# Optimization experiments

Hardware: AMD Instinct MI355X
Metric: run time of the kernel (lower is better)

## Reference

```python
import jax, jax.numpy as jnp
import numpy as np

NMS_MAX_OUTPUTS = 2000
CLS_SCORE_THRESH = 0.7
IOU_THRESH = 0.3
USE_SIDE_REFINE = False
B, N_ANCHORS, N_VALID, NUM_CLASSES = 4, 20000, 12000, 2


def setup_inputs() -> dict:
    key = jax.random.key(0)
    k = jax.random.split(key, 7)
    deltas = 0.5 * jax.random.normal(k[0], (B, N_ANCHORS, 2), jnp.float32)
    side_deltas = 0.5 * jax.random.normal(k[1], (B, N_ANCHORS, 1), jnp.float32)
    class_logits = 2.0 * jax.random.normal(k[2], (B, N_ANCHORS, NUM_CLASSES), jnp.float32)
    # CTPN-style anchors: fixed width 16, heights in [11, 280], on a ~1600px page
    cx = jax.random.uniform(k[3], (N_VALID,), jnp.float32, 8.0, 1592.0)
    cy = jax.random.uniform(k[4], (N_VALID,), jnp.float32, 0.0, 1600.0)
    h = jax.random.uniform(k[5], (N_VALID,), jnp.float32, 11.0, 280.0)
    valid_anchors = jnp.stack([cx - 8.0, cy - h * 0.5, cx + 8.0, cy + h * 0.5], axis=1)
    valid_indices = jnp.sort(
        jax.random.choice(k[6], N_ANCHORS, (N_VALID,), replace=False)
    ).astype(jnp.int32)
    return {
        "deltas": deltas,
        "side_deltas": side_deltas,
        "class_logits": class_logits,
        "valid_anchors": valid_anchors,
        "valid_indices": valid_indices,
    }


def apply_regress(deltas, side_deltas, anchors, use_side_refine):
    # deltas [B,V,2], side_deltas [B,V,1], anchors [V,4] -> [B,V,4]
    w = anchors[:, 2] - anchors[:, 0]
    h = anchors[:, 3] - anchors[:, 1]
    cx = (anchors[:, 0] + anchors[:, 2]) * 0.5
    cy = (anchors[:, 1] + anchors[:, 3]) * 0.5
    d = jnp.concatenate([deltas, side_deltas], axis=-1) * jnp.array([0.1, 0.2, 0.1], deltas.dtype)
    dy, dh, dx = d[..., 0], d[..., 1], d[..., 2]
    cy = cy + dy * h
    cx = cx + dx * w
    h = h * jnp.exp(dh)
    y1 = cy - h * 0.5
    y2 = cy + h * 0.5
    if use_side_refine:
        x1 = jnp.maximum(cx - w * 0.5, 0.0)
        x2 = cx + w * 0.5
    else:
        x1 = jnp.broadcast_to(anchors[:, 0], y1.shape)
        x2 = jnp.broadcast_to(anchors[:, 2], y1.shape)
    return jnp.stack([x1, y1, x2, y2], axis=-1)


def nms_single(boxes, scores, logits, max_out, iou_t, score_t):
    """Greedy NMS (tf.image.non_max_suppression semantics) + gather + pad_to_fixed_size."""
    V = boxes.shape[0]
    order = jnp.argsort(-jax.lax.stop_gradient(scores))
    b, s, l = boxes[order], scores[order], logits[order]
    bc = jax.lax.stop_gradient(b)  # suppression decisions are non-differentiable
    x1, y1, x2, y2 = bc[:, 0], bc[:, 1], bc[:, 2], bc[:, 3]
    areas = (x2 - x1) * (y2 - y1)
    idxs = jnp.arange(V)
    valid = jax.lax.stop_gradient(s) > score_t

    def body(i, keep):
        xx1 = jnp.maximum(x1[i], x1)
        yy1 = jnp.maximum(y1[i], y1)
        xx2 = jnp.minimum(x2[i], x2)
        yy2 = jnp.minimum(y2[i], y2)
        inter = jnp.maximum(xx2 - xx1, 0.0) * jnp.maximum(yy2 - yy1, 0.0)
        iou = inter / (areas[i] + areas - inter + 1e-10)
        sup = (iou > iou_t) & (idxs > i)
        return jnp.where(keep[i], keep & ~sup, keep)

    keep = jax.lax.fori_loop(0, V, body, valid)
    rank = jnp.cumsum(keep.astype(jnp.int32)) - 1
    sel = keep & (rank < max_out)
    dest = jnp.where(sel, rank, max_out)  # overflow rows parked at row max_out, sliced off
    tag = jnp.ones((V, 1), b.dtype)

    def pad_fixed(x):
        # append tag column of 1s for real rows, scatter to fixed size, zero-pad rest
        aug = jnp.where(sel[:, None], jnp.concatenate([x, tag], axis=1), 0.0)
        out = jnp.zeros((max_out + 1, aug.shape[1]), aug.dtype).at[dest].set(aug)
        return out[:max_out]

    return pad_fixed(b), pad_fixed(s[:, None]), pad_fixed(l)


def reference(deltas, side_deltas, class_logits, valid_anchors, valid_indices):
    d = jnp.take(deltas, valid_indices, axis=1)
    sd = jnp.take(side_deltas, valid_indices, axis=1)
    cl = jnp.take(class_logits, valid_indices, axis=1)
    class_scores = jax.nn.softmax(cl, axis=-1)
    fg_scores = jnp.max(class_scores[..., 1:], axis=-1)  # [B,V]
    proposals = apply_regress(d, sd, valid_anchors, USE_SIDE_REFINE)  # [B,V,4]
    f = lambda bb, ss, ll: nms_single(bb, ss, ll, NMS_MAX_OUTPUTS, IOU_THRESH, CLS_SCORE_THRESH)
    boxes, box_scores, out_logits = jax.vmap(f)(proposals, fg_scores, cl)
    return boxes, box_scores, out_logits
```

## Files before the change

### kernel.cpp

```cpp
#include <hip/hip_runtime.h>
#include <cstdint>
#include <cstddef>

typedef unsigned long long u64;
typedef unsigned int u32;
typedef u32 u32x4 __attribute__((ext_vector_type(4)));

#define AS1 __attribute__((address_space(1)))
#define AS3 __attribute__((address_space(3)))

constexpr int kB = 4;
constexpr int kNA = 20000;
constexpr int kV = 12000;
constexpr int kCAP = 5120;
constexpr int kW = kCAP / 64;
constexpr int kIC = 256;
constexpr int kMAXOUT = 2000;
constexpr int kGPB = 40;
constexpr float kIOU = 0.3f;
constexpr float kSCORE = 0.7f;

static __device__ __forceinline__ u64 greedy64(u64 freeS, u32 d_lo, u32 d_hi) {
  u64 keptS;
  asm volatile(
      "s_mov_b64 s[40:41], %[free]\n\t"
      "s_mov_b64 s[42:43], 0\n\t"
      "GRD_%=:\n\t"
      "s_ff1_i32_b64 s44, s[40:41]\n\t"
      "s_cmp_eq_i32 s44, -1\n\t"
      "s_cbranch_scc1 GRDEND_%=\n\t"
      "s_bitset1_b64 s[42:43], s44\n\t"
      "s_bitset0_b64 s[40:41], s44\n\t"
      "v_readlane_b32 s46, %[dlo], s44\n\t"
      "v_readlane_b32 s47, %[dhi], s44\n\t"
      "s_nop 4\n\t"
      "s_andn2_b64 s[40:41], s[40:41], s[46:47]\n\t"
      "s_branch GRD_%=\n\t"
      "GRDEND_%=:\n\t"
      "s_mov_b64 %[kept], s[42:43]\n\t"
      : [kept] "=&s"(keptS)
      : [free] "s"(freeS), [dlo] "v"(d_lo), [dhi] "v"(d_hi)
      : "s40", "s41", "s42", "s43", "s44", "s45", "s46", "s47", "scc");
  return keptS;
}

__device__ __forceinline__ u64 waveOr64(u64 v) {
  v |= __shfl_xor((unsigned long long)v, 32, 64);
  v |= __shfl_xor((unsigned long long)v, 16, 64);
  v |= __shfl_xor((unsigned long long)v, 8, 64);
  v |= __shfl_xor((unsigned long long)v, 4, 64);
  v |= __shfl_xor((unsigned long long)v, 2, 64);
  v |= __shfl_xor((unsigned long long)v, 1, 64);
  return v;
}

__global__ __launch_bounds__(256) void stage_score(
    const float* __restrict__ deltas, const float* __restrict__ logits,
    const float* __restrict__ anchors, const int* __restrict__ vidx,
    u32* __restrict__ counts, u64* __restrict__ keys,
    float* __restrict__ rec_y1, float* __restrict__ rec_y2,
    float* __restrict__ rec_l0, float* __restrict__ rec_l1) {
  int t = blockIdx.x * 256 + threadIdx.x;
  if (t >= kB * kV) return;
  int b = t / kV, i = t - b * kV;
  int lane = threadIdx.x & 63;
  int idx = vidx[i];
  float2 lg = *(const float2*)(logits + ((size_t)b * kNA + idx) * 2);
  float score = 1.0f / (1.0f + expf(lg.x - lg.y));
  if (!(score > kSCORE)) return;
  float2 dd = *(const float2*)(deltas + ((size_t)b * kNA + idx) * 2);
  float4 a = *(const float4*)(anchors + (size_t)i * 4);
  float h = a.w - a.y;
  float cy = (a.y + a.w) * 0.5f + (dd.x * 0.1f) * h;
  float hn = h * expf(dd.y * 0.2f);
  rec_y1[t] = cy - hn * 0.5f;
  rec_y2[t] = cy + hn * 0.5f;
  rec_l0[t] = lg.x;
  rec_l1[t] = lg.y;
  u64 act = __ballot(1);
  int b0 = (int)__builtin_amdgcn_readfirstlane((u32)b);
  u64 sameb = __ballot(b == b0);
  u64 grp = (b == b0) ? sameb : (act & ~sameb);
  u32 cnt = (u32)__popcll(grp);
  int lead = (int)__ffsll((unsigned long long)grp) - 1;
  u32 base = 0;
  if (lane == lead) base = atomicAdd(&counts[b], cnt);
  base = (u32)__shfl((int)base, lead, 64);
  u32 pos = base + (u32)__popcll(grp & ((1ULL << lane) - 1ULL));
  if (pos < kCAP) {
    u64 key = ((u64)(0xFFFFFFFFu - __float_as_uint(score)) << 32) | (u32)i;
    keys[(size_t)b * kCAP + pos] = key;
  }
}

__global__ __launch_bounds__(256) void rank_sort_emit(
    const u32* __restrict__ counts, const u64* __restrict__ keys,
    const float* __restrict__ rec_y1, const float* __restrict__ rec_y2,
    const float* __restrict__ rec_l0, const float* __restrict__ rec_l1,
    const float* __restrict__ anchors,
    float4* __restrict__ sbox, float* __restrict__ sarea,
    float* __restrict__ ssc, float* __restrict__ sl0, float* __restrict__ sl1) {
  __shared__ u64 sk[kCAP];
  int b = blockIdx.x / (kCAP / 256);
  int chunk = blockIdx.x % (kCAP / 256);
  int tid = threadIdx.x;
  int cnt = (int)min(counts[b], (u32)kCAP);
  for (int e = tid; e < kCAP; e += 256)
    sk[e] = (e < cnt) ? keys[(size_t)b * kCAP + e] : ~0ULL;
  __syncthreads();
  int s = chunk * 256 + tid;
  if (s >= cnt) return;
  u64 ks = sk[s];
  int rank = 0;
  for (int j = 0; j < kCAP; j += 8) {
#pragma unroll
    for (int u = 0; u < 8; ++u) rank += (sk[j + u] < ks) ? 1 : 0;
  }
  int i = (int)(u32)ks;
  float sc = __uint_as_float(0xFFFFFFFFu - (u32)(ks >> 32));
  float x1 = anchors[(size_t)i * 4 + 0], x2 = anchors[(size_t)i * 4 + 2];
  float y1 = rec_y1[b * kV + i], y2 = rec_y2[b * kV + i];
  size_t o = (size_t)b * kCAP + rank;
  sbox[o] = make_float4(x1, y1, x2, y2);
  sarea[o] = (x2 - x1) * (y2 - y1);
  ssc[o] = sc;
  sl0[o] = rec_l0[b * kV + i];
  sl1[o] = rec_l1[b * kV + i];
}

__global__ __launch_bounds__(256) void stage_mask(
    const u32* __restrict__ counts,
    const float4* __restrict__ sbox, const float* __restrict__ sarea,
    u64* __restrict__ mask) {
  __shared__ float4 sb[4][kIC];
  __shared__ float sa[4][kIC];
  int lane = threadIdx.x & 63;
  int wv = threadIdx.x >> 6;
  int gw = blockIdx.x * 4 + wv;
  int bt = gw & 3;
  int rest = gw >> 2;
  int jb = rest % kW;
  int ic = rest / kW;
  int M = (int)min(counts[bt], (u32)kCAP);
  int W = (M + 63) >> 6;
  if (jb >= W) return;
  int ibeg = ic * kIC;
  int iend = min(min(M, jb * 64 + 64), ibeg + kIC);
  if (ibeg >= iend) return;
  const float4* pb = sbox + (size_t)bt * kCAP;
  const float* pa = sarea + (size_t)bt * kCAP;
  u64* mb = mask + (size_t)bt * ((size_t)kW * kCAP);
#pragma unroll
  for (int r = 0; r < kIC / 64; ++r) {
    int e = r * 64 + lane;
    sb[wv][e] = pb[ibeg + e];
    sa[wv][e] = pa[ibeg + e];
  }
  int j = jb * 64 + lane;
  bool jv = (j < M);
  float4 bj = make_float4(0.f, 0.f, 0.f, 0.f);
  float aj = 0.f;
  if (jv) { bj = pb[j]; aj = pa[j]; }
#pragma unroll 4
  for (int i = ibeg; i < iend; ++i) {
    float4 bi = sb[wv][i - ibeg];
    float ai = sa[wv][i - ibeg];
    float xx1 = fmaxf(bi.x, bj.x);
    float yy1 = fmaxf(bi.y, bj.y);
    float xx2 = fminf(bi.z, bj.z);
    float yy2 = fminf(bi.w, bj.w);
    float inter = fmaxf(xx2 - xx1, 0.0f) * fmaxf(yy2 - yy1, 0.0f);
    float iou = inter / (ai + aj - inter + 1e-10f);
    bool sup = jv && (j > i) && (iou > kIOU);
    u64 wm = __ballot(sup);
    if (lane == 0)
      mb[(((size_t)(i >> 6)) * kW + jb) * 64 + (i & 63)] = wm;
  }
}

__global__ __launch_bounds__(64, 1) void stage_scan(
    const u32* __restrict__ counts, const u64* __restrict__ mask,
    u64* __restrict__ pub, int* __restrict__ keepidx, u32* __restrict__ kcnt) {
  __shared__ __align__(16) u64 col[80 * 128];
  const int bid = blockIdx.x;
  const int bt = bid & 3;
  const int g = bid >> 2;
  const int lane = threadIdx.x;
  const int M = (int)min(counts[bt], (u32)kCAP);
  const int W = (M + 63) >> 6;
  const int blk0 = 2 * g, blk1 = 2 * g + 1;
  if (blk0 >= W) return;
  const u64* mb = mask + (size_t)bt * ((size_t)kW * kCAP);
  u64* pp = pub + (size_t)(bt * kGPB) * 4;

#pragma unroll
  for (int b = 0; b < 80; ++b)
    __builtin_amdgcn_global_load_lds(
        (const AS1 u32*)(mb + ((size_t)b * kW + blk0) * 64 + (size_t)lane * 2),
        (AS3 u32*)&col[b * 128], 16, 0, 0);
  __builtin_amdgcn_s_waitcnt(0x0070);

  u64 acc0 = 0, acc1 = 0;
  u32 cum = 0;
  for (int w = 0; w < g; ++w) {
    const u64* q = pp + (size_t)w * 4;
    u64 km0, km1;
    for (;;) {
      u32x4 ra, rb;
      asm volatile(
          "global_load_dwordx4 %0, %2, off sc0 sc1\n\t"
          "global_load_dwordx4 %1, %2, off offset:16 sc0 sc1\n\t"
          "s_waitcnt vmcnt(0)"
          : "=v"(ra), "=v"(rb)
          : "v"(q)
          : "memory");
      u64 a0 = ((u64)ra[1] << 32) | ra[0];
      u64 a1 = ((u64)ra[3] << 32) | ra[2];
      u64 a2 = ((u64)rb[1] << 32) | rb[0];
      u64 a3 = ((u64)rb[3] << 32) | rb[2];
      if (((a0 & a1 & a2 & a3) >> 63) != 0) {
        km0 = (u64)(u32)a0 | ((u64)(u32)a1 << 32);
        km1 = (u64)(u32)a2 | ((u64)(u32)a3 << 32);
        break;
      }
      __builtin_amdgcn_s_sleep(2);
    }
    cum += (u32)__popcll(km0) + (u32)__popcll(km1);
    if (km0 | km1) {
      bool k0 = (km0 >> lane) & 1ULL, k1 = (km1 >> lane) & 1ULL;
      u64 v = (k0 ? col[(2 * w) * 128 + lane] : 0ULL) |
              (k1 ? col[(2 * w + 1) * 128 + lane] : 0ULL);
      u64 u = (k0 ? col[(2 * w) * 128 + 64 + lane] : 0ULL) |
              (k1 ? col[(2 * w + 1) * 128 + 64 + lane] : 0ULL);
      acc0 |= waveOr64(v);
      acc1 |= waveOr64(u);
    }
  }

  u64 keptm0 = 0;
  const u32 cum0 = cum;
  if ((int)cum0 < kMAXOUT) {
    int remn = M - blk0 * 64;
    u64 validm = (remn >= 64) ? ~0ULL : ((1ULL << remn) - 1ULL);
    u64 freeb = ~acc0 & validm;
    u32 flo = __builtin_amdgcn_readfirstlane((u32)freeb);
    u32 fhi = __builtin_amdgcn_readfirstlane((u32)(freeb >> 32));
    u64 diag = col[blk0 * 128 + lane];
    keptm0 = greedy64(((u64)fhi << 32) | flo, (u32)diag, (u32)(diag >> 32));
  }
  cum = cum0 + (u32)__popcll(keptm0);
  if (keptm0) {
    u64 x = ((keptm0 >> lane) & 1ULL) ? col[blk0 * 128 + 64 + lane] : 0ULL;
    acc1 |= waveOr64(x);
  }
  u64 keptm1 = 0;
  const u32 cum1 = cum;
  if (blk1 < W && (int)cum1 < kMAXOUT) {
    int remn = M - blk1 * 64;
    u64 validm = (remn >= 64) ? ~0ULL : ((1ULL << remn) - 1ULL);
    u64 freeb = ~acc1 & validm;
    u32 flo = __builtin_amdgcn_readfirstlane((u32)freeb);
    u32 fhi = __builtin_amdgcn_readfirstlane((u32)(freeb >> 32));
    u64 diag = col[blk1 * 128 + 64 + lane];
    keptm1 = greedy64(((u64)fhi << 32) | flo, (u32)diag, (u32)(diag >> 32));
  }
  cum = cum1 + (u32)__popcll(keptm1);

  if (lane == 0) {
    const u64 F = 1ULL << 63;
    (void)__hip_atomic_fetch_or(&pp[(size_t)g * 4 + 0], F | (u64)(u32)keptm0,
                                __ATOMIC_RELAXED, __HIP_MEMORY_SCOPE_AGENT);
    (void)__hip_atomic_fetch_or(&pp[(size_t)g * 4 + 1], F | (u64)(u32)(keptm0 >> 32),
                                __ATOMIC_RELAXED, __HIP_MEMORY_SCOPE_AGENT);
    (void)__hip_atomic_fetch_or(&pp[(size_t)g * 4 + 2], F | (u64)(u32)keptm1,
                                __ATOMIC_RELAXED, __HIP_MEMORY_SCOPE_AGENT);
    (void)__hip_atomic_fetch_or(&pp[(size_t)g * 4 + 3], F | (u64)(u32)(keptm1 >> 32),
                                __ATOMIC_RELAXED, __HIP_MEMORY_SCOPE_AGENT);
  }
  if ((keptm0 >> lane) & 1ULL) {
    int rank = (int)cum0 + (int)__popcll(keptm0 & ((1ULL << lane) - 1ULL));
    if (rank < kMAXOUT) keepidx[bt * kMAXOUT + rank] = blk0 * 64 + lane;
  }
  if ((keptm1 >> lane) & 1ULL) {
    int rank = (int)cum1 + (int)__popcll(keptm1 & ((1ULL << lane) - 1ULL));
    if (rank < kMAXOUT) keepidx[bt * kMAXOUT + rank] = blk1 * 64 + lane;
  }
  if (lane == 0 && g == (W - 1) / 2) kcnt[bt] = min(cum, (u32)kMAXOUT);
}

__global__ __launch_bounds__(256) void stage_out(
    const u32* __restrict__ kcnt, const int* __restrict__ keepidx,
    const float4* __restrict__ sbox, const float* __restrict__ ssc,
    const float* __restrict__ sl0, const float* __restrict__ sl1,
    float* __restrict__ out) {
  int t = blockIdx.x * 256 + threadIdx.x;
  if (t >= kB * kMAXOUT) return;
  int b = t / kMAXOUT, r = t - b * kMAXOUT;
  if (r >= (int)kcnt[b]) return;
  int i = keepidx[t];
  size_t o = (size_t)b * kCAP + i;
  float4 bx = sbox[o];
  float* boxes = out;
  float* bscores = out + (size_t)kB * kMAXOUT * 5;
  float* blogits = out + (size_t)kB * kMAXOUT * 7;
  boxes[(size_t)t * 5 + 0] = bx.x;
  boxes[(size_t)t * 5 + 1] = bx.y;
  boxes[(size_t)t * 5 + 2] = bx.z;
  boxes[(size_t)t * 5 + 3] = bx.w;
  boxes[(size_t)t * 5 + 4] = 1.0f;
  bscores[(size_t)t * 2 + 0] = ssc[o];
  bscores[(size_t)t * 2 + 1] = 1.0f;
  blogits[(size_t)t * 3 + 0] = sl0[o];
  blogits[(size_t)t * 3 + 1] = sl1[o];
  blogits[(size_t)t * 3 + 2] = 1.0f;
}

extern "C" void kernel_launch(void* const* d_in, const int* in_sizes, int n_in,
                              void* d_out, int out_size, void* d_ws, size_t ws_size,
                              hipStream_t stream) {
  const float* deltas = (const float*)d_in[0];
  const float* logits = (const float*)d_in[2];
  const float* anchors = (const float*)d_in[3];
  const int* vidx = (const int*)d_in[4];
  float* out = (float*)d_out;

  char* p = (char*)d_ws;
  auto take = [&](size_t bytes) -> char* {
    char* r = p;
    p += (bytes + 255) & ~(size_t)255;
    return r;
  };
  u32* counts = (u32*)take(kB * sizeof(u32));
  u32* kcnt = (u32*)take(kB * sizeof(u32));
  u64* pub = (u64*)take((size_t)kB * kGPB * 4 * sizeof(u64));
  u64* keys = (u64*)take((size_t)kB * kCAP * sizeof(u64));
  float* rec_y1 = (float*)take((size_t)kB * kV * sizeof(float));
  float* rec_y2 = (float*)take((size_t)kB * kV * sizeof(float));
  float* rec_l0 = (float*)take((size_t)kB * kV * sizeof(float));
  float* rec_l1 = (float*)take((size_t)kB * kV * sizeof(float));
  float4* sbox = (float4*)take((size_t)kB * kCAP * sizeof(float4));
  float* sarea = (float*)take((size_t)kB * kCAP * sizeof(float));
  float* ssc = (float*)take((size_t)kB * kCAP * sizeof(float));
  float* sl0 = (float*)take((size_t)kB * kCAP * sizeof(float));
  float* sl1 = (float*)take((size_t)kB * kCAP * sizeof(float));
  int* keepidx = (int*)take((size_t)kB * kMAXOUT * sizeof(int));
  u64* mask = (u64*)take((size_t)kB * kCAP * kW * sizeof(u64) + 4096);

  (void)hipMemsetAsync(out, 0, (size_t)out_size * sizeof(float), stream);
  (void)hipMemsetAsync(counts, 0, 5632, stream);

  stage_score<<<(kB * kV + 255) / 256, 256, 0, stream>>>(
      deltas, logits, anchors, vidx, counts, keys, rec_y1, rec_y2, rec_l0, rec_l1);
  rank_sort_emit<<<kB * (kCAP / 256), 256, 0, stream>>>(
      counts, keys, rec_y1, rec_y2, rec_l0, rec_l1, anchors,
      sbox, sarea, ssc, sl0, sl1);
  stage_mask<<<kB * kW * (kCAP / kIC) / 4, 256, 0, stream>>>(
      counts, sbox, sarea, mask);
  stage_scan<<<kB * kGPB, 64, 0, stream>>>(counts, mask, pub, keepidx, kcnt);
  stage_out<<<(kB * kMAXOUT + 255) / 256, 256, 0, stream>>>(
      kcnt, keepidx, sbox, ssc, sl0, sl1, out);
}
```

Baseline: 371.4 us.

## Rework scan-stage spin polling and block mapping to cut inter-block sync latency

```diff
diff --git a/kernel.cpp b/kernel.cpp
--- a/kernel.cpp
+++ b/kernel.cpp
@@ -183,8 +183,9 @@
     u64* __restrict__ pub, int* __restrict__ keepidx, u32* __restrict__ kcnt) {
   __shared__ __align__(16) u64 col[80 * 128];
   const int bid = blockIdx.x;
-  const int bt = bid & 3;
-  const int g = bid >> 2;
+  const int bt = bid & 7;
+  const int g = bid >> 3;
+  if (bt >= kB) return;
   const int lane = threadIdx.x;
   const int M = (int)min(counts[bt], (u32)kCAP);
   const int W = (M + 63) >> 6;
@@ -205,15 +206,22 @@
   for (int w = 0; w < g; ++w) {
     const u64* q = pp + (size_t)w * 4;
     u64 km0, km1;
+    int round = 0;
     for (;;) {
       u32x4 ra, rb;
-      asm volatile(
-          "global_load_dwordx4 %0, %2, off sc0 sc1\n\t"
-          "global_load_dwordx4 %1, %2, off offset:16 sc0 sc1\n\t"
-          "s_waitcnt vmcnt(0)"
-          : "=v"(ra), "=v"(rb)
-          : "v"(q)
-          : "memory");
+      if ((round & 7) != 7) {
+        asm volatile(
+            "global_load_dwordx4 %0, %2, off sc0\n\t"
+            "global_load_dwordx4 %1, %2, off offset:16 sc0\n\t"
+            "s_waitcnt vmcnt(0)"
+            : "=v"(ra), "=v"(rb) : "v"(q) : "memory");
+      } else {
+        asm volatile(
+            "global_load_dwordx4 %0, %2, off sc0 sc1\n\t"
+            "global_load_dwordx4 %1, %2, off offset:16 sc0 sc1\n\t"
+            "s_waitcnt vmcnt(0)"
+            : "=v"(ra), "=v"(rb) : "v"(q) : "memory");
+      }
       u64 a0 = ((u64)ra[1] << 32) | ra[0];
       u64 a1 = ((u64)ra[3] << 32) | ra[2];
       u64 a2 = ((u64)rb[1] << 32) | rb[0];
@@ -223,6 +231,7 @@
         km1 = (u64)(u32)a2 | ((u64)(u32)a3 << 32);
         break;
       }
+      ++round;
       __builtin_amdgcn_s_sleep(2);
     }
     cum += (u32)__popcll(km0) + (u32)__popcll(km1);
@@ -268,14 +277,26 @@
 
   if (lane == 0) {
     const u64 F = 1ULL << 63;
-    (void)__hip_atomic_fetch_or(&pp[(size_t)g * 4 + 0], F | (u64)(u32)keptm0,
-                                __ATOMIC_RELAXED, __HIP_MEMORY_SCOPE_AGENT);
-    (void)__hip_atomic_fetch_or(&pp[(size_t)g * 4 + 1], F | (u64)(u32)(keptm0 >> 32),
-                                __ATOMIC_RELAXED, __HIP_MEMORY_SCOPE_AGENT);
-    (void)__hip_atomic_fetch_or(&pp[(size_t)g * 4 + 2], F | (u64)(u32)keptm1,
-                                __ATOMIC_RELAXED, __HIP_MEMORY_SCOPE_AGENT);
-    (void)__hip_atomic_fetch_or(&pp[(size_t)g * 4 + 3], F | (u64)(u32)(keptm1 >> 32),
-                                __ATOMIC_RELAXED, __HIP_MEMORY_SCOPE_AGENT);
+    u64 w0 = F | (u64)(u32)keptm0;
+    u64 w1 = F | (u64)(u32)(keptm0 >> 32);
+    u64 w2 = F | (u64)(u32)keptm1;
+    u64 w3 = F | (u64)(u32)(keptm1 >> 32);
+    (void)__hip_atomic_fetch_or(&pp[(size_t)g * 4 + 0], w0, __ATOMIC_RELAXED,
+                                __HIP_MEMORY_SCOPE_WORKGROUP);
+    (void)__hip_atomic_fetch_or(&pp[(size_t)g * 4 + 1], w1, __ATOMIC_RELAXED,
+                                __HIP_MEMORY_SCOPE_WORKGROUP);
+    (void)__hip_atomic_fetch_or(&pp[(size_t)g * 4 + 2], w2, __ATOMIC_RELAXED,
+                                __HIP_MEMORY_SCOPE_WORKGROUP);
+    (void)__hip_atomic_fetch_or(&pp[(size_t)g * 4 + 3], w3, __ATOMIC_RELAXED,
+                                __HIP_MEMORY_SCOPE_WORKGROUP);
+    (void)__hip_atomic_fetch_or(&pp[(size_t)g * 4 + 0], w0, __ATOMIC_RELAXED,
+                                __HIP_MEMORY_SCOPE_AGENT);
+    (void)__hip_atomic_fetch_or(&pp[(size_t)g * 4 + 1], w1, __ATOMIC_RELAXED,
+                                __HIP_MEMORY_SCOPE_AGENT);
+    (void)__hip_atomic_fetch_or(&pp[(size_t)g * 4 + 2], w2, __ATOMIC_RELAXED,
+                                __HIP_MEMORY_SCOPE_AGENT);
+    (void)__hip_atomic_fetch_or(&pp[(size_t)g * 4 + 3], w3, __ATOMIC_RELAXED,
+                                __HIP_MEMORY_SCOPE_AGENT);
   }
   if ((keptm0 >> lane) & 1ULL) {
     int rank = (int)cum0 + (int)__popcll(keptm0 & ((1ULL << lane) - 1ULL));
@@ -356,7 +377,7 @@
       sbox, sarea, ssc, sl0, sl1);
   stage_mask<<<kB * kW * (kCAP / kIC) / 4, 256, 0, stream>>>(
       counts, sbox, sarea, mask);
-  stage_scan<<<kB * kGPB, 64, 0, stream>>>(counts, mask, pub, keepidx, kcnt);
+  stage_scan<<<kGPB * 8, 64, 0, stream>>>(counts, mask, pub, keepidx, kcnt);
   stage_out<<<(kB * kMAXOUT + 255) / 256, 256, 0, stream>>>(
       kcnt, keepidx, sbox, ssc, sl0, sl1, out);
 }
```

New measurement: 384.0 us. 1.03x slower.

## Poll all predecessor publications in one wave-wide load and trim LDS staging

Applied to the files above, without the earlier changes.

```diff
diff --git a/kernel.cpp b/kernel.cpp
--- a/kernel.cpp
+++ b/kernel.cpp
@@ -52,6 +52,12 @@
   v |= __shfl_xor((unsigned long long)v, 2, 64);
   v |= __shfl_xor((unsigned long long)v, 1, 64);
   return v;
+}
+
+__device__ __forceinline__ u64 readlane64u(u64 v, int l) {
+  u32 lo = __builtin_amdgcn_readlane((u32)v, (u32)l);
+  u32 hi = __builtin_amdgcn_readlane((u32)(v >> 32), (u32)l);
+  return ((u64)hi << 32) | lo;
 }
 
 __global__ __launch_bounds__(256) void stage_score(
@@ -193,8 +199,8 @@
   const u64* mb = mask + (size_t)bt * ((size_t)kW * kCAP);
   u64* pp = pub + (size_t)(bt * kGPB) * 4;
 
-#pragma unroll
-  for (int b = 0; b < 80; ++b)
+  const int nstage = (blk1 < 79 ? blk1 : 79) + 1;
+  for (int b = 0; b < nstage; ++b)
     __builtin_amdgcn_global_load_lds(
         (const AS1 u32*)(mb + ((size_t)b * kW + blk0) * 64 + (size_t)lane * 2),
         (AS3 u32*)&col[b * 128], 16, 0, 0);
@@ -202,39 +208,54 @@
 
   u64 acc0 = 0, acc1 = 0;
   u32 cum = 0;
-  for (int w = 0; w < g; ++w) {
-    const u64* q = pp + (size_t)w * 4;
-    u64 km0, km1;
-    for (;;) {
-      u32x4 ra, rb;
-      asm volatile(
-          "global_load_dwordx4 %0, %2, off sc0 sc1\n\t"
-          "global_load_dwordx4 %1, %2, off offset:16 sc0 sc1\n\t"
-          "s_waitcnt vmcnt(0)"
-          : "=v"(ra), "=v"(rb)
-          : "v"(q)
-          : "memory");
-      u64 a0 = ((u64)ra[1] << 32) | ra[0];
-      u64 a1 = ((u64)ra[3] << 32) | ra[2];
-      u64 a2 = ((u64)rb[1] << 32) | rb[0];
-      u64 a3 = ((u64)rb[3] << 32) | rb[2];
-      if (((a0 & a1 & a2 & a3) >> 63) != 0) {
-        km0 = (u64)(u32)a0 | ((u64)(u32)a1 << 32);
-        km1 = (u64)(u32)a2 | ((u64)(u32)a3 << 32);
-        break;
+  const u64* qa = pp + (size_t)lane * 2;
+  const u64* qb = pp + 128 + (size_t)(lane & 15) * 2;
+  int next = 0;
+  while (next < g) {
+    u32x4 ra, rb;
+    asm volatile(
+        "global_load_dwordx4 %0, %2, off sc0 sc1\n\t"
+        "global_load_dwordx4 %1, %3, off sc0 sc1\n\t"
+        "s_waitcnt vmcnt(0)"
+        : "=&v"(ra), "=&v"(rb)
+        : "v"(qa), "v"(qb)
+        : "memory");
+    u64 wA0 = ((u64)ra[1] << 32) | ra[0];
+    u64 wA1 = ((u64)ra[3] << 32) | ra[2];
+    u64 wB0 = ((u64)rb[1] << 32) | rb[0];
+    u64 wB1 = ((u64)rb[3] << 32) | rb[2];
+    u64 okA = __ballot(((wA0 & wA1) >> 63) != 0);
+    u64 okB = __ballot(((wB0 & wB1) >> 63) != 0);
+    int w = next;
+    for (; w < g; ++w) {
+      u64 km0, km1;
+      if (w < 32) {
+        if (((okA >> (2 * w)) & 3ULL) != 3ULL) break;
+        km0 = (u64)(u32)readlane64u(wA0, 2 * w) |
+              ((u64)(u32)readlane64u(wA1, 2 * w) << 32);
+        km1 = (u64)(u32)readlane64u(wA0, 2 * w + 1) |
+              ((u64)(u32)readlane64u(wA1, 2 * w + 1) << 32);
+      } else {
+        int l = 2 * (w - 32);
+        if (((okB >> l) & 3ULL) != 3ULL) break;
+        km0 = (u64)(u32)readlane64u(wB0, l) |
+              ((u64)(u32)readlane64u(wB1, l) << 32);
+        km1 = (u64)(u32)readlane64u(wB0, l + 1) |
+              ((u64)(u32)readlane64u(wB1, l + 1) << 32);
       }
-      __builtin_amdgcn_s_sleep(2);
+      cum += (u32)__popcll(km0) + (u32)__popcll(km1);
+      if (km0 | km1) {
+        bool k0 = (km0 >> lane) & 1ULL, k1 = (km1 >> lane) & 1ULL;
+        u64 v = (k0 ? col[(2 * w) * 128 + lane] : 0ULL) |
+                (k1 ? col[(2 * w + 1) * 128 + lane] : 0ULL);
+        u64 u = (k0 ? col[(2 * w) * 128 + 64 + lane] : 0ULL) |
+                (k1 ? col[(2 * w + 1) * 128 + 64 + lane] : 0ULL);
+        acc0 |= waveOr64(v);
+        acc1 |= waveOr64(u);
+      }
     }
-    cum += (u32)__popcll(km0) + (u32)__popcll(km1);
-    if (km0 | km1) {
-      bool k0 = (km0 >> lane) & 1ULL, k1 = (km1 >> lane) & 1ULL;
-      u64 v = (k0 ? col[(2 * w) * 128 + lane] : 0ULL) |
-              (k1 ? col[(2 * w + 1) * 128 + lane] : 0ULL);
-      u64 u = (k0 ? col[(2 * w) * 128 + 64 + lane] : 0ULL) |
-              (k1 ? col[(2 * w + 1) * 128 + 64 + lane] : 0ULL);
-      acc0 |= waveOr64(v);
-      acc1 |= waveOr64(u);
-    }
+    next = w;
+    if (next < g) __builtin_amdgcn_s_sleep(16);
   }
 
   u64 keptm0 = 0;
```

Measured after the change: 361.3 us. -2.7%, faster.
